# Kernel optimization log

Measured on AMD Instinct MI355X. Metric: run time of the kernel, lower is better.

## Reference

```python
import jax, jax.numpy as jnp
import numpy as np

MAX_RES = 10.0  # max_residue_magnitude

def conv3x3(x, w, b):
    # x [B,Cin,H,W], w [Cout,Cin,3,3]
    y = jax.lax.conv_general_dilated(x, w, (1, 1), 'SAME',
        dimension_numbers=('NCHW', 'OIHW', 'NCHW'))
    return y + b[None, :, None, None]

def lrelu(v):
    return jnp.where(v >= 0, v, 0.1 * v)

def setup_inputs() -> dict:
    key = jax.random.key(0)
    ks = jax.random.split(key, 12)
    B, C, H, W = 2, 64, 192, 192
    s = lambda fan: 1.0 / np.sqrt(fan)
    return {
        'x': jax.random.normal(ks[0], (B, C, H, W), jnp.float32),
        'cond_feat': jax.random.normal(ks[1], (B, 2 * C + 3, H, W), jnp.float32),
        'flow': jax.random.normal(ks[2], (B, 2, H, W), jnp.float32) * 2.0,
        'w_off1': jax.random.normal(ks[3], (C, 2 * C + 3, 3, 3), jnp.float32) * s(131 * 9),
        'b_off1': jnp.zeros((C,), jnp.float32),
        'w_off2': jax.random.normal(ks[4], (C, C, 3, 3), jnp.float32) * s(C * 9),
        'b_off2': jnp.zeros((C,), jnp.float32),
        'w_off3': jax.random.normal(ks[5], (C, C, 3, 3), jnp.float32) * s(C * 9),
        'b_off3': jnp.zeros((C,), jnp.float32),
        'w_off4': jax.random.normal(ks[6], (27, C, 3, 3), jnp.float32) * s(C * 9),
        'b_off4': jnp.zeros((27,), jnp.float32),
        'weight': jax.random.normal(ks[7], (C, C, 3, 3), jnp.float32) * s(C * 9),
        'bias': jnp.zeros((C,), jnp.float32),
    }

def deform_conv2d(x, offset, mask, weight, bias):
    # x [B,C,H,W]; offset [B,2*K,H,W] interleaved (dy,dx); mask [B,K,H,W]
    # stride=1, padding=1, dilation=1, kernel 3x3, groups=1, dg=1
    B, C, H, W = x.shape
    K = 9
    off = offset.reshape(B, K, 2, H, W)
    dy, dx = off[:, :, 0], off[:, :, 1]                 # [B,K,H,W]
    kk = jnp.arange(K)
    ky = (kk // 3).astype(jnp.float32)                  # kernel row
    kx = (kk % 3).astype(jnp.float32)                   # kernel col
    ys = jnp.arange(H, dtype=jnp.float32)
    xs = jnp.arange(W, dtype=jnp.float32)
    # sampling positions (pad=1): p = out_pos - 1 + k + offset
    py = dy + (ys[None, None, :, None] - 1.0 + ky[None, :, None, None])
    px = dx + (xs[None, None, None, :] - 1.0 + kx[None, :, None, None])

    y0 = jnp.floor(py); x0 = jnp.floor(px)
    ly = py - y0; lx = px - x0
    y0i = y0.astype(jnp.int32); x0i = x0.astype(jnp.int32)
    y1i = y0i + 1; x1i = x0i + 1

    xf = x.reshape(B, C, H * W)

    def gather(yi, xi):
        valid = (yi >= 0) & (yi < H) & (xi >= 0) & (xi < W)   # [B,K,H,W]
        yc = jnp.clip(yi, 0, H - 1)
        xc = jnp.clip(xi, 0, W - 1)
        idx = (yc * W + xc).reshape(B, -1)                    # [B,K*H*W]
        g = jax.vmap(lambda xb, ib: xb[:, ib])(xf, idx)       # [B,C,K*H*W]
        return g.reshape(B, C, K, H, W) * valid[:, None].astype(x.dtype)

    w00 = ((1 - ly) * (1 - lx))[:, None]
    w01 = ((1 - ly) * lx)[:, None]
    w10 = (ly * (1 - lx))[:, None]
    w11 = (ly * lx)[:, None]
    val = (w00 * gather(y0i, x0i) + w01 * gather(y0i, x1i)
           + w10 * gather(y1i, x0i) + w11 * gather(y1i, x1i))  # [B,C,K,H,W]
    val = val * mask[:, None]
    wr = weight.reshape(weight.shape[0], C, K)                 # [O,C,K]
    out = jnp.einsum('bckhw,ock->bohw', val, wr)
    return out + bias[None, :, None, None]

def reference(x, cond_feat, flow, w_off1, b_off1, w_off2, b_off2,
              w_off3, b_off3, w_off4, b_off4, weight, bias):
    h = lrelu(conv3x3(cond_feat, w_off1, b_off1))
    h = lrelu(conv3x3(h, w_off2, b_off2))
    h = lrelu(conv3x3(h, w_off3, b_off3))
    out = conv3x3(h, w_off4, b_off4)                           # [B,27,H,W]
    o1, o2, mask = jnp.split(out, 3, axis=1)                   # each [B,9,H,W]
    offset = MAX_RES * jnp.tanh(jnp.concatenate([o1, o2], axis=1))  # [B,18,H,W]
    flow_yx = flow[:, ::-1]                                    # flip channel dim
    offset = offset + jnp.tile(flow_yx, (1, 9, 1, 1))
    mask = jax.nn.sigmoid(mask)
    return deform_conv2d(x, offset, mask, weight, bias)
```

## Files before the change

### kernel.cpp

```cpp
#include <hip/hip_runtime.h>
#include <math.h>

#define B_ 2
#define C_ 64
#define H_ 192
#define W_ 192
#define HW_ (H_*W_)
#define PR_ 194

typedef __attribute__((ext_vector_type(8))) short    bf16x8;
typedef __attribute__((ext_vector_type(4))) float    f32x4;
typedef __attribute__((ext_vector_type(4))) unsigned u32x4;

__device__ inline unsigned short f2bf(float f) {
  unsigned u = __float_as_uint(f);
  return (unsigned short)((u + 0x7fffu + ((u >> 16) & 1u)) >> 16);
}
__device__ inline float bf2f(unsigned short h) { return __uint_as_float((unsigned)h << 16); }
__device__ inline float bflo(unsigned u) { return __uint_as_float(u << 16); }
__device__ inline float bfhi(unsigned u) { return __uint_as_float(u & 0xffff0000u); }
__device__ inline unsigned pkbf(float a, float b) {
  unsigned ua = __float_as_uint(a), ub = __float_as_uint(b);
  ua = (ua + 0x7fffu + ((ua >> 16) & 1u)) >> 16;
  ub = (ub + 0x7fffu + ((ub >> 16) & 1u)) >> 16;
  return ua | (ub << 16);
}

template<int O, int CIN, int OPAD, int CPAD>
__global__ __launch_bounds__(256) void prep_cw(const float* __restrict__ w,
                                               unsigned short* __restrict__ WH,
                                               unsigned short* __restrict__ WL)
{
  const int i = blockIdx.x * 256 + threadIdx.x;
  if (i >= 9 * OPAD * CPAD) return;
  const int k = i / (OPAD * CPAD);
  const int r = i % (OPAD * CPAD);
  const int o = r / CPAD;
  const int c = r % CPAD;
  float v = (o < O && c < CIN) ? w[((size_t)o * CIN + c) * 9 + k] : 0.f;
  const unsigned short h = f2bf(v);
  const int ot = o >> 4, l16 = o & 15;
  const int cc = c >> 5, g = (c >> 3) & 3, e = c & 7;
  const size_t off = (((((size_t)k * (OPAD / 16) + ot) * (CPAD / 32) + cc) * 16 + l16) * 4 + g) * 8 + e;
  WH[off] = h;
  WL[off] = f2bf(v - bf2f(h));
}

__global__ __launch_bounds__(256) void transpose_cond(const float* __restrict__ cond,
                                                      unsigned short* __restrict__ cH,
                                                      unsigned short* __restrict__ cL)
{
  const int tid = threadIdx.x;
  const int b  = blockIdx.x / PR_;
  const int yp = blockIdx.x % PR_;
  const int cc = blockIdx.y;
  const size_t ob = (((size_t)(b * 5 + cc) * PR_ + yp) * PR_) * 32;

  if (yp == 0 || yp == PR_ - 1) {
    u32x4 z = {0, 0, 0, 0};
    for (int idx = tid; idx < PR_ * 4; idx += 256) {
      *(u32x4*)(cH + ob + (size_t)idx * 8) = z;
      *(u32x4*)(cL + ob + (size_t)idx * 8) = z;
    }
    return;
  }
  const int y = yp - 1;
  __shared__ float t[32][PR_];

  for (int idx = tid; idx < 32 * 192; idx += 256) {
    const int ci = idx / 192, px = idx % 192;
    const int c = cc * 32 + ci;
    t[ci][px + 1] = (c < 131) ? cond[(((size_t)b * 131 + c) * H_ + y) * W_ + px] : 0.f;
  }
  if (tid < 32) { t[tid][0] = 0.f; t[tid][PR_ - 1] = 0.f; }
  __syncthreads();
  for (int idx = tid; idx < PR_ * 4; idx += 256) {
    const int px = idx >> 2, sg = idx & 3;
    u32x4 vh, vl;
    #pragma unroll
    for (int q = 0; q < 4; ++q) {
      const int c0 = sg * 8 + q * 2;
      const float va = t[c0][px], vb = t[c0 + 1][px];
      const unsigned short ha = f2bf(va), hb = f2bf(vb);
      vh[q] = (unsigned)ha | ((unsigned)hb << 16);
      const unsigned short la = f2bf(va - bf2f(ha)), lb = f2bf(vb - bf2f(hb));
      vl[q] = (unsigned)la | ((unsigned)lb << 16);
    }
    *(u32x4*)(cH + ob + (size_t)idx * 8) = vh;
    *(u32x4*)(cL + ob + (size_t)idx * 8) = vl;
  }
}

__global__ __launch_bounds__(256) void halo_zero(unsigned short* __restrict__ H,
                                                 unsigned short* __restrict__ L)
{
  const int idx = blockIdx.x * 256 + threadIdx.x;
  if (idx >= B_ * 2 * PR_ * PR_) return;
  const int r  = idx % (PR_ * PR_);
  const int yp = r / PR_, xp = r % PR_;
  if (yp == 0 || yp == PR_ - 1 || xp == 0 || xp == PR_ - 1) {
    u32x4 z = {0, 0, 0, 0};
    const size_t base = (size_t)idx * 32;
    #pragma unroll
    for (int j = 0; j < 4; ++j) {
      *(u32x4*)(H + base + j * 8) = z;
      *(u32x4*)(L + base + j * 8) = z;
    }
  }
}

template<int NCC, int NW, int EPI>
__global__ __launch_bounds__(NW * 64) void conv_mfma(
    const unsigned short* __restrict__ inH, const unsigned short* __restrict__ inL,
    const unsigned short* __restrict__ WH, const unsigned short* __restrict__ WL,
    const float* __restrict__ bias, const float* __restrict__ flow,
    unsigned short* __restrict__ outH, unsigned short* __restrict__ outL,
    float* __restrict__ om)
{
  constexpr int OPAD = NW * 16;
  const int tid = threadIdx.x;
  const int lane = tid & 63, wv = tid >> 6;
  const int g = lane >> 4, l16 = lane & 15;
  const int nwg8 = (3 * 192 * B_) / 8;
  const int t = blockIdx.x;
  const int gi = (t & 7) * nwg8 + (t >> 3);
  const int p0 = (gi % 3) * 64;
  const int y  = (gi / 3) % 192;
  const int b  = gi / 576;

  __shared__ __align__(16) unsigned short smem[3 * 4224];

  f32x4 acc[4];
  {
    float bv[4];
    #pragma unroll
    for (int r = 0; r < 4; ++r) {
      const int oc = wv * 16 + g * 4 + r;
      bv[r] = (EPI == 1 && oc >= 27) ? 0.f : bias[oc];
    }
    #pragma unroll
    for (int n = 0; n < 4; ++n) {
      acc[n][0] = bv[0]; acc[n][1] = bv[1]; acc[n][2] = bv[2]; acc[n][3] = bv[3];
    }
  }

  const int fr = l16 * 4 + g;

  for (int cc = 0; cc < NCC; ++cc) {
    __syncthreads();
    for (int ch = tid; ch < 792; ch += NW * 64) {
      const int row = ch / 264, c2 = ch % 264;
      const int px = c2 >> 2, s = c2 & 3;
      const int cg = s ^ ((px >> 1) & 3);
      const size_t so = ((((size_t)b * NCC + cc) * PR_ + (y + row)) * PR_ + p0 + px) * 32 + cg * 8;
      *(u32x4*)(smem + row * 4224 + c2 * 8)        = *(const u32x4*)(inH + so);
      *(u32x4*)(smem + row * 4224 + 2112 + c2 * 8) = *(const u32x4*)(inL + so);
    }
    __syncthreads();
    #pragma unroll
    for (int ky = 0; ky < 3; ++ky) {
      const unsigned short* stH = smem + ky * 4224;
      const unsigned short* stL = stH + 2112;
      #pragma unroll
      for (int kx = 0; kx < 3; ++kx) {
        const int k = ky * 3 + kx;
        const size_t wo = ((((size_t)k * NW + wv) * NCC + cc) * 64 + fr) * 8;
        const bf16x8 aH = *(const bf16x8*)(WH + wo);
        const bf16x8 aL = *(const bf16x8*)(WL + wo);
        #pragma unroll
        for (int n = 0; n < 4; ++n) {
          const int pxt = n * 16 + l16 + kx;
          const int bo = pxt * 32 + ((g ^ ((pxt >> 1) & 3)) * 8);
          const bf16x8 bH = *(const bf16x8*)(stH + bo);
          const bf16x8 bL = *(const bf16x8*)(stL + bo);
          acc[n] = __builtin_amdgcn_mfma_f32_16x16x32_bf16(aH, bH, acc[n], 0, 0, 0);
          acc[n] = __builtin_amdgcn_mfma_f32_16x16x32_bf16(aL, bH, acc[n], 0, 0, 0);
          acc[n] = __builtin_amdgcn_mfma_f32_16x16x32_bf16(aH, bL, acc[n], 0, 0, 0);
        }
      }
    }
  }

  if (EPI == 0) {
    __syncthreads();
    unsigned short* eH = smem;
    unsigned short* eL = smem + 64 * 72;
    #pragma unroll
    for (int n = 0; n < 4; ++n) {
      const int px = n * 16 + l16;
      #pragma unroll
      for (int r = 0; r < 4; ++r) {
        const int c = wv * 16 + g * 4 + r;
        float v = acc[n][r];
        v = (v >= 0.f) ? v : 0.1f * v;
        const unsigned short h = f2bf(v);
        eH[px * 72 + c] = h;
        eL[px * 72 + c] = f2bf(v - bf2f(h));
      }
    }
    __syncthreads();
    const int px = tid >> 2, cq = tid & 3;
    const int cc2 = cq >> 1;
    const size_t ob = ((((size_t)b * 2 + cc2) * PR_ + (y + 1)) * PR_ + (p0 + px + 1)) * 32
                    + (cq & 1) * 16;
    const u32x4 h0 = *(const u32x4*)(eH + px * 72 + cq * 16);
    const u32x4 h1 = *(const u32x4*)(eH + px * 72 + cq * 16 + 8);
    const u32x4 l0 = *(const u32x4*)(eL + px * 72 + cq * 16);
    const u32x4 l1 = *(const u32x4*)(eL + px * 72 + cq * 16 + 8);
    *(u32x4*)(outH + ob)     = h0;
    *(u32x4*)(outH + ob + 8) = h1;
    *(u32x4*)(outL + ob)     = l0;
    *(u32x4*)(outL + ob + 8) = l1;
  } else {
    #pragma unroll
    for (int n = 0; n < 4; ++n) {
      const int px = p0 + n * 16 + l16;
      #pragma unroll
      for (int r = 0; r < 4; ++r) {
        const int oc = wv * 16 + g * 4 + r;
        if (oc >= 27) continue;
        float v = acc[n][r];
        if (oc < 18) {
          const float f = flow[(((size_t)b * 2 + ((oc & 1) ? 0 : 1)) * H_ + y) * W_ + px];
          v = 10.f * tanhf(v) + f;
        } else {
          v = 1.f / (1.f + expf(-v));
        }
        om[((size_t)(b * 27 + oc) * HW_) + (size_t)y * W_ + px] = v;
      }
    }
  }
}

__global__ __launch_bounds__(256) void prep_w2(const float* __restrict__ w,
                                               unsigned short* __restrict__ W2)
{
  const int i = blockIdx.x * 256 + threadIdx.x;
  if (i < 64 * 64 * 9) {
    const int o = i / 576;
    const int rem = i % 576;
    const int c = rem / 9;
    const int k = rem % 9;
    const int wv = o >> 4, l16 = o & 15;
    const int half = c >> 5, g = (c >> 3) & 3, e = c & 7;
    const size_t off = (((((size_t)k * 4 + wv) * 2 + half) * 16 + l16) * 4 + g) * 8 + e;
    W2[off] = f2bf(w[i]);
  }
}

__global__ __launch_bounds__(256) void transpose_x(const float* __restrict__ x,
                                                   unsigned short* __restrict__ xTb)
{
  const int tid = threadIdx.x;
  const int lane = tid & 63, wv = tid >> 6;
  const int blocksPerB = HW_ / 64;
  const int b = blockIdx.x / blocksPerB;
  const int p0 = (blockIdx.x % blocksPerB) * 64;

  __shared__ float t[64][65];
  const float* xb = x + (size_t)b * C_ * HW_;
  #pragma unroll
  for (int j = 0; j < 16; ++j) {
    const int c = wv * 16 + j;
    t[c][lane] = xb[(size_t)c * HW_ + p0 + lane];
  }
  __syncthreads();
  unsigned short* xo = xTb + ((size_t)b * HW_ + p0) * 64;
  const int c4 = (tid & 15) * 4;
  const int pb = tid >> 4;
  #pragma unroll
  for (int pp = 0; pp < 4; ++pp) {
    const int p = pb + 16 * pp;
    ushort4 v = { f2bf(t[c4][p]), f2bf(t[c4+1][p]), f2bf(t[c4+2][p]), f2bf(t[c4+3][p]) };
    *(ushort4*)(xo + (size_t)p * 64 + c4) = v;
  }
}

__global__ __launch_bounds__(256) void deform_k(
    const unsigned short* __restrict__ xTb, const float* __restrict__ om,
    const unsigned short* __restrict__ W2, const float* __restrict__ bias,
    float* __restrict__ out)
{
  const int tid = threadIdx.x;
  const int lane = tid & 63, wv = tid >> 6;
  const int g = lane >> 4;
  const int l16 = lane & 15;
  const int blocksPerB = HW_ / 64;
  const int b = blockIdx.x / blocksPerB;
  const int rem = blockIdx.x % blocksPerB;
  const int h = (rem * 64) / W_;
  const int w0 = (rem * 64) % W_;

  __shared__ int   ci[4][9][64];
  __shared__ float cw[4][9][64];
  __shared__ __align__(16) unsigned short valk[64 * 64];

  for (int idx = tid; idx < 9 * 64; idx += 256) {
    const int k = idx >> 6, p = idx & 63;
    const size_t base = (size_t)b * 27 * HW_ + (size_t)h * W_ + w0 + p;
    const float dy = om[base + (size_t)(2 * k) * HW_];
    const float dx = om[base + (size_t)(2 * k + 1) * HW_];
    const float m  = om[base + (size_t)(18 + k) * HW_];
    const int ky = k / 3, kx = k - ky * 3;
    const float py = dy + (float)(h - 1 + ky);
    const float px = dx + (float)(w0 + p - 1 + kx);
    const float y0f = floorf(py), x0f = floorf(px);
    const float ly = py - y0f, lx = px - x0f;
    const int y0 = (int)y0f, x0 = (int)x0f;
    const int y1 = y0 + 1, x1 = x0 + 1;
    float w00 = (1.f - ly) * (1.f - lx), w01 = (1.f - ly) * lx;
    float w10 = ly * (1.f - lx),        w11 = ly * lx;
    if (!(y0 >= 0 && y0 < H_)) { w00 = 0.f; w01 = 0.f; }
    if (!(y1 >= 0 && y1 < H_)) { w10 = 0.f; w11 = 0.f; }
    if (!(x0 >= 0 && x0 < W_)) { w00 = 0.f; w10 = 0.f; }
    if (!(x1 >= 0 && x1 < W_)) { w01 = 0.f; w11 = 0.f; }
    const int yc0 = min(max(y0, 0), H_ - 1), yc1 = min(max(y1, 0), H_ - 1);
    const int xc0 = min(max(x0, 0), W_ - 1), xc1 = min(max(x1, 0), W_ - 1);
    ci[0][k][p] = yc0 * W_ + xc0;  cw[0][k][p] = m * w00;
    ci[1][k][p] = yc0 * W_ + xc1;  cw[1][k][p] = m * w01;
    ci[2][k][p] = yc1 * W_ + xc0;  cw[2][k][p] = m * w10;
    ci[3][k][p] = yc1 * W_ + xc1;  cw[3][k][p] = m * w11;
  }

  f32x4 acc[4];
  {
    float br[4];
    #pragma unroll
    for (int r = 0; r < 4; ++r) br[r] = bias[wv * 16 + g * 4 + r];
    #pragma unroll
    for (int n = 0; n < 4; ++n) { acc[n][0]=br[0]; acc[n][1]=br[1]; acc[n][2]=br[2]; acc[n][3]=br[3]; }
  }

  const unsigned short* xb = xTb + (size_t)b * HW_ * 64;
  const int fr = l16 * 4 + g;
  __syncthreads();

  for (int k = 0; k < 9; ++k) {
    #pragma unroll
    for (int i = 0; i < 2; ++i) {
      const int it = tid + (i << 8);
      const int cg = it & 7, p = it >> 3;
      const int i00 = ci[0][k][p], i01 = ci[1][k][p];
      const int i10 = ci[2][k][p], i11 = ci[3][k][p];
      const float q00 = cw[0][k][p], q01 = cw[1][k][p];
      const float q10 = cw[2][k][p], q11 = cw[3][k][p];
      const u32x4 va = *(const u32x4*)(xb + ((size_t)i00 * 64 + cg * 8));
      const u32x4 vb = *(const u32x4*)(xb + ((size_t)i01 * 64 + cg * 8));
      const u32x4 vc = *(const u32x4*)(xb + ((size_t)i10 * 64 + cg * 8));
      const u32x4 vd = *(const u32x4*)(xb + ((size_t)i11 * 64 + cg * 8));
      u32x4 res;
      #pragma unroll
      for (int j = 0; j < 4; ++j) {
        const float lo = q00*bflo(va[j]) + q01*bflo(vb[j]) + q10*bflo(vc[j]) + q11*bflo(vd[j]);
        const float hi = q00*bfhi(va[j]) + q01*bfhi(vb[j]) + q10*bfhi(vc[j]) + q11*bfhi(vd[j]);
        res[j] = pkbf(lo, hi);
      }
      *(u32x4*)&valk[(p << 6) + ((cg ^ (p & 7)) << 3)] = res;
    }

    const size_t wb = ((((size_t)k * 4 + wv) * 2) * 64 + fr) * 8;
    const bf16x8 a0 = *(const bf16x8*)(W2 + wb);
    const bf16x8 a1 = *(const bf16x8*)(W2 + wb + 512);

    __syncthreads();

    #pragma unroll
    for (int n = 0; n < 4; ++n) {
      const int p = n * 16 + l16;
      const bf16x8 b0 = *(const bf16x8*)&valk[(p << 6) + (((g    ) ^ (p & 7)) << 3)];
      const bf16x8 b1 = *(const bf16x8*)&valk[(p << 6) + (((g + 4) ^ (p & 7)) << 3)];
      acc[n] = __builtin_amdgcn_mfma_f32_16x16x32_bf16(a0, b0, acc[n], 0, 0, 0);
      acc[n] = __builtin_amdgcn_mfma_f32_16x16x32_bf16(a1, b1, acc[n], 0, 0, 0);
    }
    __syncthreads();
  }

  #pragma unroll
  for (int n = 0; n < 4; ++n) {
    #pragma unroll
    for (int r = 0; r < 4; ++r) {
      const int oc = wv * 16 + g * 4 + r;
      out[((size_t)(b * C_ + oc) * HW_) + (size_t)h * W_ + w0 + n * 16 + l16] = acc[n][r];
    }
  }
}

extern "C" void kernel_launch(void* const* d_in, const int* in_sizes, int n_in,
                              void* d_out, int out_size, void* d_ws, size_t ws_size,
                              hipStream_t stream) {
  const float* x         = (const float*)d_in[0];
  const float* cond_feat = (const float*)d_in[1];
  const float* flow      = (const float*)d_in[2];
  const float* w1 = (const float*)d_in[3];  const float* b1 = (const float*)d_in[4];
  const float* w2 = (const float*)d_in[5];  const float* b2 = (const float*)d_in[6];
  const float* w3 = (const float*)d_in[7];  const float* b3 = (const float*)d_in[8];
  const float* w4 = (const float*)d_in[9];  const float* b4 = (const float*)d_in[10];
  const float* wgt = (const float*)d_in[11]; const float* bias = (const float*)d_in[12];

  float* outp = (float*)d_out;

  char* wsp = (char*)d_ws;
  size_t off = 0;
  auto alloc = [&](size_t bytes) { char* p = wsp + off; off += (bytes + 255) & ~(size_t)255; return p; };
  const size_t padHW = (size_t)PR_ * PR_;
  unsigned short* condH = (unsigned short*)alloc(B_ * 5 * padHW * 32 * 2);
  unsigned short* condL = (unsigned short*)alloc(B_ * 5 * padHW * 32 * 2);
  unsigned short* hA_H  = (unsigned short*)alloc(B_ * 2 * padHW * 32 * 2);
  unsigned short* hA_L  = (unsigned short*)alloc(B_ * 2 * padHW * 32 * 2);
  unsigned short* hB_H  = (unsigned short*)alloc(B_ * 2 * padHW * 32 * 2);
  unsigned short* hB_L  = (unsigned short*)alloc(B_ * 2 * padHW * 32 * 2);
  float*          om    = (float*)alloc((size_t)B_ * 27 * HW_ * 4);
  unsigned short* xTb   = (unsigned short*)alloc((size_t)B_ * HW_ * 64 * 2);
  unsigned short* W2d   = (unsigned short*)alloc(9 * 64 * 64 * 2);
  unsigned short* W1H   = (unsigned short*)alloc(9 * 64 * 160 * 2);
  unsigned short* W1L   = (unsigned short*)alloc(9 * 64 * 160 * 2);
  unsigned short* W2H   = (unsigned short*)alloc(9 * 64 * 64 * 2);
  unsigned short* W2L   = (unsigned short*)alloc(9 * 64 * 64 * 2);
  unsigned short* W3H   = (unsigned short*)alloc(9 * 64 * 64 * 2);
  unsigned short* W3L   = (unsigned short*)alloc(9 * 64 * 64 * 2);
  unsigned short* W4H   = (unsigned short*)alloc(9 * 32 * 64 * 2);
  unsigned short* W4L   = (unsigned short*)alloc(9 * 32 * 64 * 2);

  prep_cw<64, 131, 64, 160><<<(9*64*160 + 255)/256, 256, 0, stream>>>(w1, W1H, W1L);
  prep_cw<64, 64, 64, 64><<<(9*64*64 + 255)/256, 256, 0, stream>>>(w2, W2H, W2L);
  prep_cw<64, 64, 64, 64><<<(9*64*64 + 255)/256, 256, 0, stream>>>(w3, W3H, W3L);
  prep_cw<27, 64, 32, 64><<<(9*32*64 + 255)/256, 256, 0, stream>>>(w4, W4H, W4L);
  prep_w2<<<144, 256, 0, stream>>>(wgt, W2d);

  transpose_cond<<<dim3(B_ * PR_, 5), 256, 0, stream>>>(cond_feat, condH, condL);
  halo_zero<<<(B_ * 2 * PR_ * PR_ + 255)/256, 256, 0, stream>>>(hA_H, hA_L);
  halo_zero<<<(B_ * 2 * PR_ * PR_ + 255)/256, 256, 0, stream>>>(hB_H, hB_L);
  transpose_x<<<(B_ * HW_)/64, 256, 0, stream>>>(x, xTb);

  const int nwg = 3 * 192 * B_;
  conv_mfma<5, 4, 0><<<nwg, 256, 0, stream>>>(condH, condL, W1H, W1L, b1, nullptr, hA_H, hA_L, nullptr);
  conv_mfma<2, 4, 0><<<nwg, 256, 0, stream>>>(hA_H, hA_L, W2H, W2L, b2, nullptr, hB_H, hB_L, nullptr);
  conv_mfma<2, 4, 0><<<nwg, 256, 0, stream>>>(hB_H, hB_L, W3H, W3L, b3, nullptr, hA_H, hA_L, nullptr);
  conv_mfma<2, 2, 1><<<nwg, 128, 0, stream>>>(hA_H, hA_L, W4H, W4L, b4, flow, nullptr, nullptr, om);

  deform_k<<<(B_ * HW_)/64, 256, 0, stream>>>(xTb, om, W2d, bias, outp);
}
```

Measured before the change: 185.3 us.

## Switch conv kernels to 32x32x16 MFMA with pixel-split waves over 96-pixel tiles

The 3x3 conv kernels now use 32x32x16 bf16 MFMA instead of 16x16x32. Each of three waves owns 32 pixels and loops over all output-channel tiles, so B fragments are reused across output tiles and weights are re-read per wave. Tiles grow from 64 to 96 pixels, which reduces halo overhead and the number of blocks. The weight prep layout is changed to match the new A-fragment layout. In exchange, more accumulator registers are used (up to 32 floats per tile) and fewer blocks are launched.

```diff
diff --git a/kernel.cpp b/kernel.cpp
--- a/kernel.cpp
+++ b/kernel.cpp
@@ -8,9 +8,10 @@
 #define HW_ (H_*W_)
 #define PR_ 194
 
-typedef __attribute__((ext_vector_type(8))) short    bf16x8;
-typedef __attribute__((ext_vector_type(4))) float    f32x4;
-typedef __attribute__((ext_vector_type(4))) unsigned u32x4;
+typedef __attribute__((ext_vector_type(8)))  short    bf16x8;
+typedef __attribute__((ext_vector_type(4)))  float    f32x4;
+typedef __attribute__((ext_vector_type(16))) float    f32x16;
+typedef __attribute__((ext_vector_type(4)))  unsigned u32x4;
 
 __device__ inline unsigned short f2bf(float f) {
   unsigned u = __float_as_uint(f);
@@ -39,9 +40,10 @@
   const int c = r % CPAD;
   float v = (o < O && c < CIN) ? w[((size_t)o * CIN + c) * 9 + k] : 0.f;
   const unsigned short h = f2bf(v);
-  const int ot = o >> 4, l16 = o & 15;
-  const int cc = c >> 5, g = (c >> 3) & 3, e = c & 7;
-  const size_t off = (((((size_t)k * (OPAD / 16) + ot) * (CPAD / 32) + cc) * 16 + l16) * 4 + g) * 8 + e;
+  const int ot = o >> 5, ocl = o & 31;
+  const int cc = c >> 5, ks = (c >> 4) & 1, kh = (c >> 3) & 1, e = c & 7;
+  const int lane2 = ocl + 32 * kh;
+  const size_t off = (((((size_t)k * (OPAD / 32) + ot) * (CPAD / 32) + cc) * 2 + ks) * 64 + lane2) * 8 + e;
   WH[off] = h;
   WL[off] = f2bf(v - bf2f(h));
 }
@@ -109,73 +111,73 @@
   }
 }
 
-template<int NCC, int NW, int EPI>
-__global__ __launch_bounds__(NW * 64) void conv_mfma(
+template<int NCC, int WOC, int EPI>
+__global__ __launch_bounds__(192) void conv_mfma(
     const unsigned short* __restrict__ inH, const unsigned short* __restrict__ inL,
     const unsigned short* __restrict__ WH, const unsigned short* __restrict__ WL,
     const float* __restrict__ bias, const float* __restrict__ flow,
     unsigned short* __restrict__ outH, unsigned short* __restrict__ outL,
     float* __restrict__ om)
 {
-  constexpr int OPAD = NW * 16;
   const int tid = threadIdx.x;
   const int lane = tid & 63, wv = tid >> 6;
-  const int g = lane >> 4, l16 = lane & 15;
-  const int nwg8 = (3 * 192 * B_) / 8;
+  const int l32 = lane & 31, lh = lane >> 5;
+  const int nwg8 = (2 * 192 * B_) / 8;
   const int t = blockIdx.x;
   const int gi = (t & 7) * nwg8 + (t >> 3);
-  const int p0 = (gi % 3) * 64;
-  const int y  = (gi / 3) % 192;
-  const int b  = gi / 576;
-
-  __shared__ __align__(16) unsigned short smem[3 * 4224];
-
-  f32x4 acc[4];
-  {
-    float bv[4];
-    #pragma unroll
-    for (int r = 0; r < 4; ++r) {
-      const int oc = wv * 16 + g * 4 + r;
-      bv[r] = (EPI == 1 && oc >= 27) ? 0.f : bias[oc];
-    }
-    #pragma unroll
-    for (int n = 0; n < 4; ++n) {
-      acc[n][0] = bv[0]; acc[n][1] = bv[1]; acc[n][2] = bv[2]; acc[n][3] = bv[3];
-    }
-  }
-
-  const int fr = l16 * 4 + g;
+  const int p0 = (gi % 2) * 96;
+  const int y  = (gi / 2) % 192;
+  const int b  = gi / 384;
+
+  __shared__ __align__(16) unsigned short smem[3 * 2 * 3136];
+
+  f32x16 acc[WOC];
+  #pragma unroll
+  for (int ot = 0; ot < WOC; ++ot)
+    #pragma unroll
+    for (int r = 0; r < 16; ++r) {
+      const int oc = ot * 32 + (r & 3) + 8 * (r >> 2) + 4 * lh;
+      acc[ot][r] = (EPI == 1 && oc >= 27) ? 0.f : bias[oc];
+    }
 
   for (int cc = 0; cc < NCC; ++cc) {
     __syncthreads();
-    for (int ch = tid; ch < 792; ch += NW * 64) {
-      const int row = ch / 264, c2 = ch % 264;
-      const int px = c2 >> 2, s = c2 & 3;
+    for (int idx = tid; idx < 1176; idx += 192) {
+      const int row = idx / 392, rem = idx % 392;
+      const int px = rem >> 2, s = rem & 3;
       const int cg = s ^ ((px >> 1) & 3);
       const size_t so = ((((size_t)b * NCC + cc) * PR_ + (y + row)) * PR_ + p0 + px) * 32 + cg * 8;
-      *(u32x4*)(smem + row * 4224 + c2 * 8)        = *(const u32x4*)(inH + so);
-      *(u32x4*)(smem + row * 4224 + 2112 + c2 * 8) = *(const u32x4*)(inL + so);
+      *(u32x4*)(smem + (row * 2 + 0) * 3136 + rem * 8) = *(const u32x4*)(inH + so);
+      *(u32x4*)(smem + (row * 2 + 1) * 3136 + rem * 8) = *(const u32x4*)(inL + so);
     }
     __syncthreads();
     #pragma unroll
     for (int ky = 0; ky < 3; ++ky) {
-      const unsigned short* stH = smem + ky * 4224;
-      const unsigned short* stL = stH + 2112;
+      const unsigned short* stH = smem + (ky * 2 + 0) * 3136;
+      const unsigned short* stL = smem + (ky * 2 + 1) * 3136;
       #pragma unroll
       for (int kx = 0; kx < 3; ++kx) {
         const int k = ky * 3 + kx;
-        const size_t wo = ((((size_t)k * NW + wv) * NCC + cc) * 64 + fr) * 8;
-        const bf16x8 aH = *(const bf16x8*)(WH + wo);
-        const bf16x8 aL = *(const bf16x8*)(WL + wo);
+        const int pxt = wv * 32 + l32 + kx;
+        bf16x8 bH[2], bL[2];
         #pragma unroll
-        for (int n = 0; n < 4; ++n) {
-          const int pxt = n * 16 + l16 + kx;
-          const int bo = pxt * 32 + ((g ^ ((pxt >> 1) & 3)) * 8);
-          const bf16x8 bH = *(const bf16x8*)(stH + bo);
-          const bf16x8 bL = *(const bf16x8*)(stL + bo);
-          acc[n] = __builtin_amdgcn_mfma_f32_16x16x32_bf16(aH, bH, acc[n], 0, 0, 0);
-          acc[n] = __builtin_amdgcn_mfma_f32_16x16x32_bf16(aL, bH, acc[n], 0, 0, 0);
-          acc[n] = __builtin_amdgcn_mfma_f32_16x16x32_bf16(aH, bL, acc[n], 0, 0, 0);
+        for (int ks = 0; ks < 2; ++ks) {
+          const int cg = ks * 2 + lh;
+          const int bo = (pxt * 4 + (cg ^ ((pxt >> 1) & 3))) * 8;
+          bH[ks] = *(const bf16x8*)(stH + bo);
+          bL[ks] = *(const bf16x8*)(stL + bo);
+        }
+        #pragma unroll
+        for (int ot = 0; ot < WOC; ++ot) {
+          #pragma unroll
+          for (int ks = 0; ks < 2; ++ks) {
+            const size_t wo = (((((size_t)k * WOC + ot) * NCC + cc) * 2 + ks) * 64 + lane) * 8;
+            const bf16x8 aH = *(const bf16x8*)(WH + wo);
+            const bf16x8 aL = *(const bf16x8*)(WL + wo);
+            acc[ot] = __builtin_amdgcn_mfma_f32_32x32x16_bf16(aH, bH[ks], acc[ot], 0, 0, 0);
+            acc[ot] = __builtin_amdgcn_mfma_f32_32x32x16_bf16(aL, bH[ks], acc[ot], 0, 0, 0);
+            acc[ot] = __builtin_amdgcn_mfma_f32_32x32x16_bf16(aH, bL[ks], acc[ot], 0, 0, 0);
+          }
         }
       }
     }
@@ -184,50 +186,44 @@
   if (EPI == 0) {
     __syncthreads();
     unsigned short* eH = smem;
-    unsigned short* eL = smem + 64 * 72;
-    #pragma unroll
-    for (int n = 0; n < 4; ++n) {
-      const int px = n * 16 + l16;
+    unsigned short* eL = smem + 6912;
+    const int px = wv * 32 + l32;
+    #pragma unroll
+    for (int ot = 0; ot < WOC; ++ot)
       #pragma unroll
-      for (int r = 0; r < 4; ++r) {
-        const int c = wv * 16 + g * 4 + r;
-        float v = acc[n][r];
+      for (int r = 0; r < 16; ++r) {
+        const int c = ot * 32 + (r & 3) + 8 * (r >> 2) + 4 * lh;
+        float v = acc[ot][r];
         v = (v >= 0.f) ? v : 0.1f * v;
         const unsigned short h = f2bf(v);
         eH[px * 72 + c] = h;
         eL[px * 72 + c] = f2bf(v - bf2f(h));
       }
-    }
-    __syncthreads();
-    const int px = tid >> 2, cq = tid & 3;
-    const int cc2 = cq >> 1;
-    const size_t ob = ((((size_t)b * 2 + cc2) * PR_ + (y + 1)) * PR_ + (p0 + px + 1)) * 32
-                    + (cq & 1) * 16;
-    const u32x4 h0 = *(const u32x4*)(eH + px * 72 + cq * 16);
-    const u32x4 h1 = *(const u32x4*)(eH + px * 72 + cq * 16 + 8);
-    const u32x4 l0 = *(const u32x4*)(eL + px * 72 + cq * 16);
-    const u32x4 l1 = *(const u32x4*)(eL + px * 72 + cq * 16 + 8);
-    *(u32x4*)(outH + ob)     = h0;
-    *(u32x4*)(outH + ob + 8) = h1;
-    *(u32x4*)(outL + ob)     = l0;
-    *(u32x4*)(outL + ob + 8) = l1;
+    __syncthreads();
+    for (int idx = tid; idx < 384; idx += 192) {
+      const int pxo = idx >> 2, cq = idx & 3;
+      const int cc2 = cq >> 1;
+      const size_t ob = ((((size_t)b * 2 + cc2) * PR_ + (y + 1)) * PR_ + (p0 + pxo + 1)) * 32
+                      + (cq & 1) * 16;
+      *(u32x4*)(outH + ob)     = *(const u32x4*)(eH + pxo * 72 + cq * 16);
+      *(u32x4*)(outH + ob + 8) = *(const u32x4*)(eH + pxo * 72 + cq * 16 + 8);
+      *(u32x4*)(outL + ob)     = *(const u32x4*)(eL + pxo * 72 + cq * 16);
+      *(u32x4*)(outL + ob + 8) = *(const u32x4*)(eL + pxo * 72 + cq * 16 + 8);
+    }
   } else {
-    #pragma unroll
-    for (int n = 0; n < 4; ++n) {
-      const int px = p0 + n * 16 + l16;
-      #pragma unroll
-      for (int r = 0; r < 4; ++r) {
-        const int oc = wv * 16 + g * 4 + r;
-        if (oc >= 27) continue;
-        float v = acc[n][r];
-        if (oc < 18) {
-          const float f = flow[(((size_t)b * 2 + ((oc & 1) ? 0 : 1)) * H_ + y) * W_ + px];
-          v = 10.f * tanhf(v) + f;
-        } else {
-          v = 1.f / (1.f + expf(-v));
-        }
-        om[((size_t)(b * 27 + oc) * HW_) + (size_t)y * W_ + px] = v;
+    const int px = p0 + wv * 32 + l32;
+    #pragma unroll
+    for (int r = 0; r < 16; ++r) {
+      const int oc = (r & 3) + 8 * (r >> 2) + 4 * lh;
+      if (oc >= 27) continue;
+      float v = acc[0][r];
+      if (oc < 18) {
+        const float f = flow[(((size_t)b * 2 + ((oc & 1) ? 0 : 1)) * H_ + y) * W_ + px];
+        v = 10.f * tanhf(v) + f;
+      } else {
+        v = 1.f / (1.f + expf(-v));
       }
+      om[((size_t)(b * 27 + oc) * HW_) + (size_t)y * W_ + px] = v;
     }
   }
 }
@@ -432,11 +428,11 @@
   halo_zero<<<(B_ * 2 * PR_ * PR_ + 255)/256, 256, 0, stream>>>(hB_H, hB_L);
   transpose_x<<<(B_ * HW_)/64, 256, 0, stream>>>(x, xTb);
 
-  const int nwg = 3 * 192 * B_;
-  conv_mfma<5, 4, 0><<<nwg, 256, 0, stream>>>(condH, condL, W1H, W1L, b1, nullptr, hA_H, hA_L, nullptr);
-  conv_mfma<2, 4, 0><<<nwg, 256, 0, stream>>>(hA_H, hA_L, W2H, W2L, b2, nullptr, hB_H, hB_L, nullptr);
-  conv_mfma<2, 4, 0><<<nwg, 256, 0, stream>>>(hB_H, hB_L, W3H, W3L, b3, nullptr, hA_H, hA_L, nullptr);
-  conv_mfma<2, 2, 1><<<nwg, 128, 0, stream>>>(hA_H, hA_L, W4H, W4L, b4, flow, nullptr, nullptr, om);
+  const int nwg = 2 * 192 * B_;
+  conv_mfma<5, 2, 0><<<nwg, 192, 0, stream>>>(condH, condL, W1H, W1L, b1, nullptr, hA_H, hA_L, nullptr);
+  conv_mfma<2, 2, 0><<<nwg, 192, 0, stream>>>(hA_H, hA_L, W2H, W2L, b2, nullptr, hB_H, hB_L, nullptr);
+  conv_mfma<2, 2, 0><<<nwg, 192, 0, stream>>>(hB_H, hB_L, W3H, W3L, b3, nullptr, hA_H, hA_L, nullptr);
+  conv_mfma<2, 1, 1><<<nwg, 192, 0, stream>>>(hA_H, hA_L, W4H, W4L, b4, flow, nullptr, nullptr, om);
 
   deform_k<<<(B_ * HW_)/64, 256, 0, stream>>>(xTb, om, W2d, bias, outp);
 }
```

New measurement: 237.9 us. 28.4% more time.

## Reuse shared-memory B fragments across kx via shifted accumulators

Applied to the files above, without the earlier changes.

Loads each input fragment from LDS once per kernel row and applies all three kx weight taps to it, accumulating into three separate accumulator sets. The shifted partial sums are combined through an LDS staging buffer, with extra masked MFMAs covering halo columns at tile edges. This cuts LDS read traffic per MFMA. In exchange it triples accumulator registers, adds barriers, and makes the offset/mask epilogue a per-pixel serial loop over channels.

```diff
diff --git a/kernel.cpp b/kernel.cpp
--- a/kernel.cpp
+++ b/kernel.cpp
@@ -117,7 +117,6 @@
     unsigned short* __restrict__ outH, unsigned short* __restrict__ outL,
     float* __restrict__ om)
 {
-  constexpr int OPAD = NW * 16;
   const int tid = threadIdx.x;
   const int lane = tid & 63, wv = tid >> 6;
   const int g = lane >> 4, l16 = lane & 15;
@@ -130,7 +129,7 @@
 
   __shared__ __align__(16) unsigned short smem[3 * 4224];
 
-  f32x4 acc[4];
+  f32x4 accC[4], accP[4], accM[4];
   {
     float bv[4];
     #pragma unroll
@@ -140,7 +139,9 @@
     }
     #pragma unroll
     for (int n = 0; n < 4; ++n) {
-      acc[n][0] = bv[0]; acc[n][1] = bv[1]; acc[n][2] = bv[2]; acc[n][3] = bv[3];
+      accC[n][0] = bv[0]; accC[n][1] = bv[1]; accC[n][2] = bv[2]; accC[n][3] = bv[3];
+      accP[n][0] = 0.f; accP[n][1] = 0.f; accP[n][2] = 0.f; accP[n][3] = 0.f;
+      accM[n][0] = 0.f; accM[n][1] = 0.f; accM[n][2] = 0.f; accM[n][3] = 0.f;
     }
   }
 
@@ -161,72 +162,123 @@
     for (int ky = 0; ky < 3; ++ky) {
       const unsigned short* stH = smem + ky * 4224;
       const unsigned short* stL = stH + 2112;
+      bf16x8 aH[3], aL[3];
       #pragma unroll
       for (int kx = 0; kx < 3; ++kx) {
         const int k = ky * 3 + kx;
         const size_t wo = ((((size_t)k * NW + wv) * NCC + cc) * 64 + fr) * 8;
-        const bf16x8 aH = *(const bf16x8*)(WH + wo);
-        const bf16x8 aL = *(const bf16x8*)(WL + wo);
-        #pragma unroll
-        for (int n = 0; n < 4; ++n) {
-          const int pxt = n * 16 + l16 + kx;
-          const int bo = pxt * 32 + ((g ^ ((pxt >> 1) & 3)) * 8);
-          const bf16x8 bH = *(const bf16x8*)(stH + bo);
-          const bf16x8 bL = *(const bf16x8*)(stL + bo);
-          acc[n] = __builtin_amdgcn_mfma_f32_16x16x32_bf16(aH, bH, acc[n], 0, 0, 0);
-          acc[n] = __builtin_amdgcn_mfma_f32_16x16x32_bf16(aL, bH, acc[n], 0, 0, 0);
-          acc[n] = __builtin_amdgcn_mfma_f32_16x16x32_bf16(aH, bL, acc[n], 0, 0, 0);
-        }
-      }
-    }
-  }
+        aH[kx] = *(const bf16x8*)(WH + wo);
+        aL[kx] = *(const bf16x8*)(WL + wo);
+      }
+      #pragma unroll
+      for (int n = 0; n < 4; ++n) {
+        const int pxt = n * 16 + l16 + 1;
+        const int bo = pxt * 32 + ((g ^ ((pxt >> 1) & 3)) * 8);
+        const bf16x8 bH = *(const bf16x8*)(stH + bo);
+        const bf16x8 bL = *(const bf16x8*)(stL + bo);
+        accP[n] = __builtin_amdgcn_mfma_f32_16x16x32_bf16(aH[0], bH, accP[n], 0, 0, 0);
+        accP[n] = __builtin_amdgcn_mfma_f32_16x16x32_bf16(aL[0], bH, accP[n], 0, 0, 0);
+        accP[n] = __builtin_amdgcn_mfma_f32_16x16x32_bf16(aH[0], bL, accP[n], 0, 0, 0);
+        accC[n] = __builtin_amdgcn_mfma_f32_16x16x32_bf16(aH[1], bH, accC[n], 0, 0, 0);
+        accC[n] = __builtin_amdgcn_mfma_f32_16x16x32_bf16(aL[1], bH, accC[n], 0, 0, 0);
+        accC[n] = __builtin_amdgcn_mfma_f32_16x16x32_bf16(aH[1], bL, accC[n], 0, 0, 0);
+        accM[n] = __builtin_amdgcn_mfma_f32_16x16x32_bf16(aH[2], bH, accM[n], 0, 0, 0);
+        accM[n] = __builtin_amdgcn_mfma_f32_16x16x32_bf16(aL[2], bH, accM[n], 0, 0, 0);
+        accM[n] = __builtin_amdgcn_mfma_f32_16x16x32_bf16(aH[2], bL, accM[n], 0, 0, 0);
+      }
+      {
+        const bf16x8 z = {0, 0, 0, 0, 0, 0, 0, 0};
+        bf16x8 xh0 = *(const bf16x8*)(stH + g * 8);
+        bf16x8 xl0 = *(const bf16x8*)(stL + g * 8);
+        xh0 = (l16 == 0) ? xh0 : z;  xl0 = (l16 == 0) ? xl0 : z;
+        accC[0] = __builtin_amdgcn_mfma_f32_16x16x32_bf16(aH[0], xh0, accC[0], 0, 0, 0);
+        accC[0] = __builtin_amdgcn_mfma_f32_16x16x32_bf16(aL[0], xh0, accC[0], 0, 0, 0);
+        accC[0] = __builtin_amdgcn_mfma_f32_16x16x32_bf16(aH[0], xl0, accC[0], 0, 0, 0);
+        bf16x8 xh1 = *(const bf16x8*)(stH + 65 * 32 + g * 8);
+        bf16x8 xl1 = *(const bf16x8*)(stL + 65 * 32 + g * 8);
+        xh1 = (l16 == 15) ? xh1 : z;  xl1 = (l16 == 15) ? xl1 : z;
+        accC[3] = __builtin_amdgcn_mfma_f32_16x16x32_bf16(aH[2], xh1, accC[3], 0, 0, 0);
+        accC[3] = __builtin_amdgcn_mfma_f32_16x16x32_bf16(aL[2], xh1, accC[3], 0, 0, 0);
+        accC[3] = __builtin_amdgcn_mfma_f32_16x16x32_bf16(aH[2], xl1, accC[3], 0, 0, 0);
+      }
+    }
+  }
+
+  __syncthreads();
+  float* fbuf = (float*)smem;
+  const int cbase = wv * 16 + g * 4;
+  #pragma unroll
+  for (int n = 0; n < 4; ++n)
+    *(f32x4*)(fbuf + (size_t)(n * 16 + l16) * 76 + cbase) = accC[n];
+  __syncthreads();
+  #pragma unroll
+  for (int n = 0; n < 4; ++n) {
+    const int o = n * 16 + l16 + 1;
+    if (o < 64) {
+      f32x4* p = (f32x4*)(fbuf + (size_t)o * 76 + cbase);
+      f32x4 v = *p;
+      v[0] += accP[n][0]; v[1] += accP[n][1]; v[2] += accP[n][2]; v[3] += accP[n][3];
+      *p = v;
+    }
+  }
+  __syncthreads();
+  #pragma unroll
+  for (int n = 0; n < 4; ++n) {
+    const int o = n * 16 + l16 - 1;
+    if (o >= 0) {
+      f32x4* p = (f32x4*)(fbuf + (size_t)o * 76 + cbase);
+      f32x4 v = *p;
+      v[0] += accM[n][0]; v[1] += accM[n][1]; v[2] += accM[n][2]; v[3] += accM[n][3];
+      *p = v;
+    }
+  }
+  __syncthreads();
 
   if (EPI == 0) {
-    __syncthreads();
-    unsigned short* eH = smem;
-    unsigned short* eL = smem + 64 * 72;
-    #pragma unroll
-    for (int n = 0; n < 4; ++n) {
-      const int px = n * 16 + l16;
+    const int px = tid >> 2, cq = tid & 3;
+    const float* src = fbuf + (size_t)px * 76 + cq * 16;
+    float w[16];
+    #pragma unroll
+    for (int i = 0; i < 4; ++i) {
+      const f32x4 v = *(const f32x4*)(src + i * 4);
       #pragma unroll
       for (int r = 0; r < 4; ++r) {
-        const int c = wv * 16 + g * 4 + r;
-        float v = acc[n][r];
-        v = (v >= 0.f) ? v : 0.1f * v;
-        const unsigned short h = f2bf(v);
-        eH[px * 72 + c] = h;
-        eL[px * 72 + c] = f2bf(v - bf2f(h));
-      }
-    }
-    __syncthreads();
-    const int px = tid >> 2, cq = tid & 3;
-    const int cc2 = cq >> 1;
-    const size_t ob = ((((size_t)b * 2 + cc2) * PR_ + (y + 1)) * PR_ + (p0 + px + 1)) * 32
+        const float x = v[r];
+        w[i * 4 + r] = (x >= 0.f) ? x : 0.1f * x;
+      }
+    }
+    u32x4 H0, H1, L0, L1;
+    #pragma unroll
+    for (int j = 0; j < 4; ++j) {
+      const float a0 = w[2 * j], b0 = w[2 * j + 1];
+      const unsigned short ha = f2bf(a0), hb = f2bf(b0);
+      H0[j] = (unsigned)ha | ((unsigned)hb << 16);
+      const unsigned short la = f2bf(a0 - bf2f(ha)), lb = f2bf(b0 - bf2f(hb));
+      L0[j] = (unsigned)la | ((unsigned)lb << 16);
+      const float a1 = w[8 + 2 * j], b1 = w[9 + 2 * j];
+      const unsigned short ha1 = f2bf(a1), hb1 = f2bf(b1);
+      H1[j] = (unsigned)ha1 | ((unsigned)hb1 << 16);
+      const unsigned short la1 = f2bf(a1 - bf2f(ha1)), lb1 = f2bf(b1 - bf2f(hb1));
+      L1[j] = (unsigned)la1 | ((unsigned)lb1 << 16);
+    }
+    const size_t ob = ((((size_t)b * 2 + (cq >> 1)) * PR_ + (y + 1)) * PR_ + (p0 + px + 1)) * 32
                     + (cq & 1) * 16;
-    const u32x4 h0 = *(const u32x4*)(eH + px * 72 + cq * 16);
-    const u32x4 h1 = *(const u32x4*)(eH + px * 72 + cq * 16 + 8);
-    const u32x4 l0 = *(const u32x4*)(eL + px * 72 + cq * 16);
-    const u32x4 l1 = *(const u32x4*)(eL + px * 72 + cq * 16 + 8);
-    *(u32x4*)(outH + ob)     = h0;
-    *(u32x4*)(outH + ob + 8) = h1;
-    *(u32x4*)(outL + ob)     = l0;
-    *(u32x4*)(outL + ob + 8) = l1;
+    *(u32x4*)(outH + ob)     = H0;
+    *(u32x4*)(outH + ob + 8) = H1;
+    *(u32x4*)(outL + ob)     = L0;
+    *(u32x4*)(outL + ob + 8) = L1;
   } else {
-    #pragma unroll
-    for (int n = 0; n < 4; ++n) {
-      const int px = p0 + n * 16 + l16;
-      #pragma unroll
-      for (int r = 0; r < 4; ++r) {
-        const int oc = wv * 16 + g * 4 + r;
-        if (oc >= 27) continue;
-        float v = acc[n][r];
+    for (int px = tid; px < 64; px += NW * 64) {
+      #pragma unroll 1
+      for (int oc = 0; oc < 27; ++oc) {
+        float v = fbuf[(size_t)px * 76 + oc];
         if (oc < 18) {
-          const float f = flow[(((size_t)b * 2 + ((oc & 1) ? 0 : 1)) * H_ + y) * W_ + px];
+          const float f = flow[(((size_t)b * 2 + ((oc & 1) ? 0 : 1)) * H_ + y) * W_ + p0 + px];
           v = 10.f * tanhf(v) + f;
         } else {
           v = 1.f / (1.f + expf(-v));
         }
-        om[((size_t)(b * 27 + oc) * HW_) + (size_t)y * W_ + px] = v;
+        om[((size_t)(b * 27 + oc) * HW_) + (size_t)y * W_ + p0 + px] = v;
       }
     }
   }
```

New measurement: 208.1 us. 12.3% more time.
